# Kernel tuning notes

Hardware: AMD Instinct MI355X
Metric: run time of the kernel (lower is better)

Reference implementation:

```python
import jax, jax.numpy as jnp
import numpy as np
import math

B, S, D = 2, 2048, 1024
H, HKV, HD = 16, 4, 64
SF = 4
SD = HD // SF  # sparsity proj dim = 16
TEMP = 1.0
INIT_STD = 0.02


def rope(qk):
    # qk: [b, h, s, d]
    d = qk.shape[-1]
    theta = 1.0 / (10000.0 ** (jnp.arange(0, d, 2, dtype=jnp.float32) / d))  # [d/2]
    s = jnp.arange(qk.shape[2], dtype=jnp.float32)
    freqs = jnp.outer(s, theta)                     # [s, d/2]
    freqs = jnp.concatenate([freqs, freqs], -1)     # [s, d]
    qk1, qk2 = jnp.split(qk, 2, axis=-1)
    rot = jnp.concatenate([-qk2, qk1], -1)
    return qk * jnp.cos(freqs) + rot * jnp.sin(freqs)


def setup_inputs() -> dict:
    key = jax.random.key(0)
    ks = jax.random.split(key, 8)
    x = jax.random.normal(ks[0], (B, S, D), dtype=jnp.float32)
    Wq = jax.random.normal(ks[1], (D, D), dtype=jnp.float32) * INIT_STD
    Wk = jax.random.normal(ks[2], (HKV * HD, D), dtype=jnp.float32) * INIT_STD
    Wv = jax.random.normal(ks[3], (HKV * HD, D), dtype=jnp.float32) * INIT_STD
    Wo = jax.random.normal(ks[4], (D, D), dtype=jnp.float32) * INIT_STD
    bo = jnp.zeros((D,), dtype=jnp.float32)
    Ws = jax.random.normal(ks[5], (SD, HD), dtype=jnp.float32) * INIT_STD
    bs = jnp.zeros((SD,), dtype=jnp.float32)
    return {"x": x, "Wq": Wq, "Wk": Wk, "Wv": Wv, "Wo": Wo, "bo": bo, "Ws": Ws, "bs": bs}


def reference(x, Wq, Wk, Wv, Wo, bo, Ws, bs):
    b, s, _ = x.shape
    # projections (torch Linear: x @ W.T)
    q = (x @ Wq.T).reshape(b, s, H, HD).transpose(0, 2, 1, 3)     # [b,H,s,hd]
    k = (x @ Wk.T).reshape(b, s, HKV, HD).transpose(0, 2, 1, 3)   # [b,Hkv,s,hd]
    v = (x @ Wv.T).reshape(b, s, HKV, HD).transpose(0, 2, 1, 3)
    q = rope(q)
    k = rope(k)
    n_rep = H // HKV
    k = jnp.repeat(k, n_rep, axis=1)  # [b,H,s,hd]
    v = jnp.repeat(v, n_rep, axis=1)
    # low-rank sparsity gate
    q_sp = q @ Ws.T + bs              # [b,H,s,sd]
    k_sp = k @ Ws.T + bs
    sp_scores = jnp.einsum('bhid,bhjd->bhij', q_sp, k_sp) / math.sqrt(SD)
    gate = jax.nn.sigmoid(sp_scores / TEMP)
    attn = jnp.einsum('bhid,bhjd->bhij', q, k) / math.sqrt(HD)
    attn = attn * gate
    causal = jnp.triu(jnp.ones((s, s), dtype=bool), k=1)
    attn = jnp.where(causal, -jnp.inf, attn)
    w = jax.nn.softmax(attn, axis=-1)
    out = jnp.einsum('bhij,bhjd->bhid', w, v)               # [b,H,s,hd]
    out = out.transpose(0, 2, 1, 3).reshape(b, s, H * HD)   # [b,s,D]
    return out @ Wo.T + bo
```

## Files before the change

kernel.cpp:

```cpp
#include <hip/hip_runtime.h>
#include <math.h>

#define B_ 2
#define S_ 2048
#define D_ 1024
#define H_ 16
#define HKV_ 4
#define HD_ 64
#define SD_ 16

typedef __attribute__((ext_vector_type(8))) short bf16x8;
typedef __attribute__((ext_vector_type(4))) float f32x4;
typedef __attribute__((ext_vector_type(8))) unsigned short us8;
typedef __attribute__((ext_vector_type(4))) unsigned short us4;

#define LOG2E 1.4426950408889634f

__device__ __forceinline__ unsigned short f2bf(float f) {
  unsigned int u = __builtin_bit_cast(unsigned int, f);
  u += 0x7fffu + ((u >> 16) & 1u);
  return (unsigned short)(u >> 16);
}

__device__ __forceinline__ void gload16(const unsigned short* g, unsigned short* l) {
  __builtin_amdgcn_global_load_lds(
      (const __attribute__((address_space(1))) unsigned int*)g,
      (__attribute__((address_space(3))) unsigned int*)l, 16, 0, 0);
}

__global__ __launch_bounds__(256) void convert_bf16(
    const float* __restrict__ x, const float* __restrict__ wq,
    const float* __restrict__ wk, const float* __restrict__ wv,
    const float* __restrict__ wo, unsigned short* __restrict__ xb,
    unsigned short* __restrict__ wqkv, unsigned short* __restrict__ wob) {
  const int blk = blockIdx.x;
  const float* src;
  unsigned short* dst;
  int off;
  if (blk < 2048)      { src = x;  dst = xb;             off = blk * 2048; }
  else if (blk < 2560) { src = wq; dst = wqkv;           off = (blk - 2048) * 2048; }
  else if (blk < 2688) { src = wk; dst = wqkv + 1048576; off = (blk - 2560) * 2048; }
  else if (blk < 2816) { src = wv; dst = wqkv + 1310720; off = (blk - 2688) * 2048; }
  else                 { src = wo; dst = wob;            off = (blk - 2816) * 2048; }
  const int i = off + threadIdx.x * 8;
  float4 a = *(const float4*)(src + i);
  float4 b = *(const float4*)(src + i + 4);
  us8 o;
  o[0] = f2bf(a.x); o[1] = f2bf(a.y); o[2] = f2bf(a.z); o[3] = f2bf(a.w);
  o[4] = f2bf(b.x); o[5] = f2bf(b.y); o[6] = f2bf(b.z); o[7] = f2bf(b.w);
  *(us8*)(dst + i) = o;
}

__global__ __launch_bounds__(256) void gemm_bf16(
    const unsigned short* __restrict__ A, const unsigned short* __restrict__ Bm,
    const float* __restrict__ bias, float* __restrict__ C, int N) {
  __shared__ unsigned short As[64 * 64];
  __shared__ unsigned short Bs[128 * 64];
  const int tid = threadIdx.x;
  const int w = tid >> 6, lane = tid & 63;
  const int nm = lane & 15, quad = lane >> 4;
  const int m0 = blockIdx.y * 64, n0 = blockIdx.x * 128;
  const int wn = w * 32;

  f32x4 acc[4][2] = {};
  int arow[2], acol[2], brow[4], bcol[4];
#pragma unroll
  for (int it = 0; it < 2; ++it) {
    int s = it * 256 + tid;
    arow[it] = s >> 3;
    acol[it] = ((s & 7) ^ (arow[it] & 7)) * 8;
  }
#pragma unroll
  for (int it = 0; it < 4; ++it) {
    int s = it * 256 + tid;
    brow[it] = s >> 3;
    bcol[it] = ((s & 7) ^ (brow[it] & 7)) * 8;
  }

  for (int k0 = 0; k0 < 1024; k0 += 64) {
    __syncthreads();
#pragma unroll
    for (int it = 0; it < 2; ++it)
      gload16(A + (size_t)(m0 + arow[it]) * 1024 + k0 + acol[it],
              &As[(it * 256 + w * 64) * 8]);
#pragma unroll
    for (int it = 0; it < 4; ++it)
      gload16(Bm + (size_t)(n0 + brow[it]) * 1024 + k0 + bcol[it],
              &Bs[(it * 256 + w * 64) * 8]);
    __syncthreads();

#pragma unroll
    for (int ks = 0; ks < 2; ++ks) {
      const int cq = ks * 4 + quad;
      bf16x8 af[4], bfr[2];
#pragma unroll
      for (int mi = 0; mi < 4; ++mi) {
        const int m = mi * 16 + nm;
        af[mi] = *(const bf16x8*)&As[(m * 8 + (cq ^ (m & 7))) * 8];
      }
#pragma unroll
      for (int ni = 0; ni < 2; ++ni) {
        const int n = wn + ni * 16 + nm;
        bfr[ni] = *(const bf16x8*)&Bs[(n * 8 + (cq ^ (n & 7))) * 8];
      }
#pragma unroll
      for (int mi = 0; mi < 4; ++mi)
#pragma unroll
        for (int ni = 0; ni < 2; ++ni)
          acc[mi][ni] = __builtin_amdgcn_mfma_f32_16x16x32_bf16(
              af[mi], bfr[ni], acc[mi][ni], 0, 0, 0);
    }
  }

  float bv[2] = {0.f, 0.f};
  if (bias) {
#pragma unroll
    for (int ni = 0; ni < 2; ++ni) bv[ni] = bias[n0 + wn + ni * 16 + nm];
  }
#pragma unroll
  for (int mi = 0; mi < 4; ++mi) {
#pragma unroll
    for (int r = 0; r < 4; ++r) {
      const int row = m0 + mi * 16 + quad * 4 + r;
      float* crow = C + (size_t)row * N + n0 + wn + nm;
#pragma unroll
      for (int ni = 0; ni < 2; ++ni) crow[ni * 16] = acc[mi][ni][r] + bv[ni];
    }
  }
}

__global__ __launch_bounds__(256) void rope_scatter(
    const float* __restrict__ P, const float* __restrict__ Ws,
    const float* __restrict__ bs, unsigned short* __restrict__ qh,
    unsigned short* __restrict__ kh, unsigned short* __restrict__ qsp,
    unsigned short* __restrict__ ksp) {
  __shared__ float wsl[16 * 64];
  __shared__ float bsl[16];
  __shared__ float rbuf[4][64];
  const int tid = threadIdx.x;
  const int row = blockIdx.x;
  const int b = row >> 11;
  const int s = row & 2047;
  {
    *(float4*)&wsl[tid * 4] = *(const float4*)&Ws[tid * 4];
    if (tid < 16) bsl[tid] = bs[tid];
  }
  __syncthreads();
  const int w = tid >> 6, lane = tid & 63;
  const int i = lane & 31, halfu = lane >> 5;
  const float theta = powf(10000.f, -((float)(2 * i) * (1.f / 64.f)));
  const float f = (float)s * theta;
  const float cf = cosf(f);
  const float sf = sinf(f);
  for (int slot = w; slot < 20; slot += 4) {
    float val = P[(size_t)row * 1536 + slot * 64 + lane];
    float partner = __shfl_xor(val, 32);
    float rot = halfu ? partner : -partner;
    float r = val * cf + rot * sf;
    unsigned short* dst;
    unsigned short* spdst;
    float qscale, spscale;
    if (slot < 16) {
      dst = qh + ((size_t)(b * 16 + slot) * 2048 + s) * 64;
      spdst = qsp + ((size_t)(b * 16 + slot) * 2048 + s) * 16;
      qscale = 0.125f * LOG2E; spscale = 0.25f * LOG2E;
    } else {
      int hh = slot - 16;
      dst = kh + ((size_t)(b * 4 + hh) * 2048 + s) * 64;
      spdst = ksp + ((size_t)(b * 4 + hh) * 2048 + s) * 16;
      qscale = 1.f; spscale = 1.f;
    }
    dst[lane] = f2bf(r * qscale);
    rbuf[w][lane] = r;
    int p = lane >> 4, j = lane & 15;
    float partial = 0.f;
#pragma unroll
    for (int t = 0; t < 16; ++t)
      partial += wsl[j * 64 + p * 16 + t] * rbuf[w][p * 16 + t];
    partial += __shfl_xor(partial, 16);
    partial += __shfl_xor(partial, 32);
    if (p == 0) spdst[j] = f2bf((partial + bsl[j]) * spscale);
  }
}

__global__ __launch_bounds__(256) void v_transpose(
    const float* __restrict__ proj, unsigned short* __restrict__ vt) {
  __shared__ unsigned short t_[64 * 72];
  const int bkv = blockIdx.y;
  const int s0 = blockIdx.x * 64;
  const int b = bkv >> 2, hkv = bkv & 3;
  const int tid = threadIdx.x;
  const int sl = tid >> 2;
  const int c0 = (tid & 3) * 16;
  const float* src = proj + ((size_t)b * 2048 + s0 + sl) * 1536 + 1280 + hkv * 64 + c0;
  us8 o0, o1;
#pragma unroll
  for (int t = 0; t < 8; ++t) { o0[t] = f2bf(src[t]); o1[t] = f2bf(src[8 + t]); }
  *(us8*)&t_[sl * 72 + c0] = o0;
  *(us8*)&t_[sl * 72 + c0 + 8] = o1;
  __syncthreads();
  const int d = tid >> 2;
  const int sc_ = (tid & 3) * 16;
  us8 w0, w1;
#pragma unroll
  for (int t = 0; t < 8; ++t) w0[t] = t_[(sc_ + t) * 72 + d];
#pragma unroll
  for (int t = 0; t < 8; ++t) w1[t] = t_[(sc_ + 8 + t) * 72 + d];
  unsigned short* dst = vt + (size_t)bkv * 131072 + (size_t)d * 2048 + s0 + sc_;
  *(us8*)dst = w0;
  *(us8*)(dst + 8) = w1;
}

template <bool MASK>
__device__ __forceinline__ void attn_tile(
    const unsigned short* __restrict__ Ksb, const unsigned short* __restrict__ Vsb,
    const unsigned short* __restrict__ Kspb_, unsigned short* __restrict__ pt,
    bf16x8 qa0, bf16x8 qa1, bf16x8 qspa, int j0, int qrow0, int nm, int quad,
    int ws, float& l_q, f32x4 O[4]) {
#pragma unroll
  for (int stl = 0; stl < 2; ++stl) {
    const int st = ws * 2 + stl;
    const int kg0 = j0 + st * 16;
    unsigned short* wptr = &pt[nm * 32 + (((stl * 4 + quad) ^ (nm & 6)) * 4)];
    if (MASK && (kg0 > qrow0 + 15)) {
      uint2 zz; zz.x = 0u; zz.y = 0u;
      *(uint2*)wptr = zz;
      continue;
    }
    const int krow = st * 16 + nm;
    const int r7 = krow & 7;
    bf16x8 kb0 = *(const bf16x8*)&Ksb[(krow * 8 + (quad ^ r7)) * 8];
    bf16x8 kb1 = *(const bf16x8*)&Ksb[(krow * 8 + ((4 + quad) ^ r7)) * 8];
    bf16x8 gb = *(const bf16x8*)&Kspb_[(krow * 2 + (quad & 1)) * 8];
    f32x4 z = {0.f, 0.f, 0.f, 0.f};
    f32x4 s = __builtin_amdgcn_mfma_f32_16x16x32_bf16(kb0, qa0, z, 0, 0, 0);
    s = __builtin_amdgcn_mfma_f32_16x16x32_bf16(kb1, qa1, s, 0, 0, 0);
    f32x4 g = __builtin_amdgcn_mfma_f32_16x16x32_bf16(gb, qspa, z, 0, 0, 0);
    const int qv = qrow0 + nm;
    float p0, p1, p2, p3;
#pragma unroll
    for (int r = 0; r < 4; ++r) {
      float gate = __builtin_amdgcn_rcpf(1.f + __builtin_amdgcn_exp2f(-g[r]));
      float v = s[r] * gate;
      if (MASK && (kg0 + 15 > qrow0)) {
        const int key = kg0 + quad * 4 + r;
        v = (key > qv) ? -INFINITY : v;
      }
      float p = __builtin_amdgcn_exp2f(v);
      l_q += p;
      if (r == 0) p0 = p; else if (r == 1) p1 = p; else if (r == 2) p2 = p; else p3 = p;
    }
    unsigned int u0 = (unsigned int)f2bf(p0) | ((unsigned int)f2bf(p1) << 16);
    unsigned int u1 = (unsigned int)f2bf(p2) | ((unsigned int)f2bf(p3) << 16);
    uint2 pk; pk.x = u0; pk.y = u1;
    *(uint2*)wptr = pk;
  }

  bf16x8 pa = *(const bf16x8*)&pt[nm * 32 + (((quad * 2) ^ (nm & 6)) * 4)];
#pragma unroll
  for (int dt = 0; dt < 4; ++dt) {
    const int vrow = dt * 16 + nm;
    bf16x8 vb = *(const bf16x8*)&Vsb[(vrow * 8 + ((ws * 4 + quad) ^ (vrow & 7))) * 8];
    O[dt] = __builtin_amdgcn_mfma_f32_16x16x32_bf16(pa, vb, O[dt], 0, 0, 0);
  }
}

__global__ __launch_bounds__(512) void attn_kernel(
    const unsigned short* __restrict__ qh, const unsigned short* __restrict__ kh,
    const unsigned short* __restrict__ vt, const unsigned short* __restrict__ qsp,
    const unsigned short* __restrict__ ksp, unsigned short* __restrict__ ao) {
  __shared__ unsigned short Ks[2][64 * 64];
  __shared__ unsigned short Vs[2][64 * 64];
  __shared__ unsigned short Ksp[2][64 * 16];
  __shared__ unsigned short Pt[8][512];
  __shared__ float Ox[4][16][64];
  __shared__ float Lxs[4][2][16];

  const int tid = threadIdx.x;
  const int w = tid >> 6;
  const int ws = w >> 2;
  const int wr = w & 3;
  const int lane = tid & 63;
  const int nm = lane & 15;
  const int quad = lane >> 4;
  const int bh = blockIdx.y;
  const int b = bh >> 4, h = bh & 15;
  const int hkv = h >> 2;
  const size_t kbase = (size_t)(b * 4 + hkv) * 2048 * 64;
  const size_t vbase = (size_t)(b * 4 + hkv) * 131072;
  const size_t kspb = (size_t)(b * 4 + hkv) * 2048 * 16;

  const int Lc = tid;
  const int sr = Lc >> 3;
  const int sc = ((Lc & 7) ^ (sr & 7)) * 8;
  unsigned short* pt = &Pt[w][0];

#define STAGE(BUF, J0)                                                         \
  {                                                                            \
    gload16(kh + kbase + (size_t)((J0) + sr) * 64 + sc,                        \
            &Ks[BUF][(w * 64) * 8]);                                           \
    gload16(vt + vbase + (size_t)sr * 2048 + (J0) + sc,                        \
            &Vs[BUF][(w * 64) * 8]);                                           \
    if (w < 2) {                                                               \
      gload16(ksp + kspb + (size_t)((J0) + (Lc >> 1)) * 16 + (Lc & 1) * 8,     \
              &Ksp[BUF][w * 512]);                                             \
    }                                                                          \
  }

  const int qxA = 31 - blockIdx.x;
  const int qxB = blockIdx.x;
  const int qrow0A = qxA * 64 + wr * 16;
  const int qrow0B = qxB * 64 + wr * 16;

  const size_t qbA = ((size_t)(b * 16 + h) * 2048 + qrow0A + nm) * 64;
  bf16x8 qa0A = *(const bf16x8*)(qh + qbA + quad * 8);
  bf16x8 qa1A = *(const bf16x8*)(qh + qbA + 32 + quad * 8);
  const size_t qbB = ((size_t)(b * 16 + h) * 2048 + qrow0B + nm) * 64;
  bf16x8 qa0B = *(const bf16x8*)(qh + qbB + quad * 8);
  bf16x8 qa1B = *(const bf16x8*)(qh + qbB + 32 + quad * 8);
  bf16x8 qspaA = {0, 0, 0, 0, 0, 0, 0, 0};
  bf16x8 qspaB = {0, 0, 0, 0, 0, 0, 0, 0};
  if (quad < 2) {
    qspaA = *(const bf16x8*)(qsp + ((size_t)(b * 16 + h) * 2048 + qrow0A + nm) * 16 + quad * 8);
    qspaB = *(const bf16x8*)(qsp + ((size_t)(b * 16 + h) * 2048 + qrow0B + nm) * 16 + quad * 8);
  }

  float l_q = 0.f;
  f32x4 O[4] = {{0.f, 0.f, 0.f, 0.f}, {0.f, 0.f, 0.f, 0.f},
                {0.f, 0.f, 0.f, 0.f}, {0.f, 0.f, 0.f, 0.f}};

  STAGE(0, 0);
  int cur = 0;
  for (int jt = 0; jt < qxA; ++jt) {
    __syncthreads();
    STAGE(cur ^ 1, (jt + 1) * 64)
    attn_tile<false>(&Ks[cur][0], &Vs[cur][0], &Ksp[cur][0], pt,
                     qa0A, qa1A, qspaA, jt * 64, qrow0A, nm, quad, ws, l_q, O);
    cur ^= 1;
  }
  __syncthreads();
  STAGE(cur ^ 1, 0)
  attn_tile<true>(&Ks[cur][0], &Vs[cur][0], &Ksp[cur][0], pt,
                  qa0A, qa1A, qspaA, qxA * 64, qrow0A, nm, quad, ws, l_q, O);
  cur ^= 1;

  {
    float lsum = l_q;
    lsum += __shfl_xor(lsum, 16);
    lsum += __shfl_xor(lsum, 32);
    if (quad == 0) Lxs[wr][ws][nm] = lsum;
  }
  if (ws == 1) {
#pragma unroll
    for (int dt = 0; dt < 4; ++dt)
#pragma unroll
      for (int r = 0; r < 4; ++r) Ox[wr][dt * 4 + r][lane] = O[dt][r];
  }
  __syncthreads();
  if (ws == 0) {
#pragma unroll
    for (int r = 0; r < 4; ++r) {
      const float tot = Lxs[wr][0][quad * 4 + r] + Lxs[wr][1][quad * 4 + r];
      const float inv = __builtin_amdgcn_rcpf(tot);
      const int rowg = qrow0A + quad * 4 + r;
      unsigned short* orow = ao + ((size_t)b * 2048 + rowg) * 1024 + h * 64 + nm;
#pragma unroll
      for (int dt = 0; dt < 4; ++dt)
        orow[dt * 16] = f2bf((O[dt][r] + Ox[wr][dt * 4 + r][lane]) * inv);
    }
  }
#pragma unroll
  for (int dt = 0; dt < 4; ++dt) O[dt] = (f32x4){0.f, 0.f, 0.f, 0.f};
  l_q = 0.f;

  for (int jt = 0; jt < qxB; ++jt) {
    __syncthreads();
    STAGE(cur ^ 1, (jt + 1) * 64)
    attn_tile<false>(&Ks[cur][0], &Vs[cur][0], &Ksp[cur][0], pt,
                     qa0B, qa1B, qspaB, jt * 64, qrow0B, nm, quad, ws, l_q, O);
    cur ^= 1;
  }
  __syncthreads();
  attn_tile<true>(&Ks[cur][0], &Vs[cur][0], &Ksp[cur][0], pt,
                  qa0B, qa1B, qspaB, qxB * 64, qrow0B, nm, quad, ws, l_q, O);

  {
    float lsum = l_q;
    lsum += __shfl_xor(lsum, 16);
    lsum += __shfl_xor(lsum, 32);
    if (quad == 0) Lxs[wr][ws][nm] = lsum;
  }
  if (ws == 1) {
#pragma unroll
    for (int dt = 0; dt < 4; ++dt)
#pragma unroll
      for (int r = 0; r < 4; ++r) Ox[wr][dt * 4 + r][lane] = O[dt][r];
  }
  __syncthreads();
  if (ws == 0) {
#pragma unroll
    for (int r = 0; r < 4; ++r) {
      const float tot = Lxs[wr][0][quad * 4 + r] + Lxs[wr][1][quad * 4 + r];
      const float inv = __builtin_amdgcn_rcpf(tot);
      const int rowg = qrow0B + quad * 4 + r;
      unsigned short* orow = ao + ((size_t)b * 2048 + rowg) * 1024 + h * 64 + nm;
#pragma unroll
      for (int dt = 0; dt < 4; ++dt)
        orow[dt * 16] = f2bf((O[dt][r] + Ox[wr][dt * 4 + r][lane]) * inv);
    }
  }
#undef STAGE
}

extern "C" void kernel_launch(void* const* d_in, const int* in_sizes, int n_in,
                              void* d_out, int out_size, void* d_ws,
                              size_t ws_size, hipStream_t stream) {
  const float* x = (const float*)d_in[0];
  const float* Wq = (const float*)d_in[1];
  const float* Wk = (const float*)d_in[2];
  const float* Wv = (const float*)d_in[3];
  const float* Wo = (const float*)d_in[4];
  const float* bo = (const float*)d_in[5];
  const float* Ws = (const float*)d_in[6];
  const float* bs = (const float*)d_in[7];
  float* out = (float*)d_out;

  char* wsb = (char*)d_ws;
  float* proj = (float*)wsb;
  unsigned short* aob  = (unsigned short*)wsb;
  unsigned short* qh   = (unsigned short*)(wsb + 25165824);
  unsigned short* kh   = (unsigned short*)(wsb + 33554432);
  unsigned short* vtb  = (unsigned short*)(wsb + 35651584);
  unsigned short* qsp  = (unsigned short*)(wsb + 37748736);
  unsigned short* ksp  = (unsigned short*)(wsb + 39845888);
  unsigned short* xb   = (unsigned short*)(wsb + 40370176);
  unsigned short* wqkv = (unsigned short*)(wsb + 48758784);
  unsigned short* wob  = (unsigned short*)(wsb + 51904512);

  convert_bf16<<<dim3(3328), 256, 0, stream>>>(x, Wq, Wk, Wv, Wo, xb, wqkv, wob);
  gemm_bf16<<<dim3(12, 64), 256, 0, stream>>>(xb, wqkv, nullptr, proj, 1536);
  rope_scatter<<<dim3(4096), 256, 0, stream>>>(proj, Ws, bs, qh, kh, qsp, ksp);
  v_transpose<<<dim3(32, 8), 256, 0, stream>>>(proj, vtb);
  attn_kernel<<<dim3(16, 32), 512, 0, stream>>>(qh, kh, vtb, qsp, ksp, aob);
  gemm_bf16<<<dim3(8, 64), 256, 0, stream>>>(aob, wob, bo, out, 1024);
}
```

Baseline: 189.4 us.

## Triple-buffer K/V staging with vmcnt waits and fuse both query-tile loops

Replaces the double-buffered K/V/Ksp staging with a three-stage ring and merges the two query-tile passes into one 33-iteration loop, so loads run two tiles ahead across the pass boundary. Waiting on outstanding loads now uses explicit s_waitcnt vmcnt counts plus a raw s_barrier instead of __syncthreads. The Ox cross-wave reduction buffer is dropped and its data written into the consumed K/V slot, which offsets the extra LDS taken by the third stage. The hand-tuned vmcnt counts depend on exactly how many loads each wave issues per STAGE, so they are fragile if the load mix changes.

```diff
diff --git a/kernel.cpp b/kernel.cpp
--- a/kernel.cpp
+++ b/kernel.cpp
@@ -269,11 +269,10 @@
     const unsigned short* __restrict__ qh, const unsigned short* __restrict__ kh,
     const unsigned short* __restrict__ vt, const unsigned short* __restrict__ qsp,
     const unsigned short* __restrict__ ksp, unsigned short* __restrict__ ao) {
-  __shared__ unsigned short Ks[2][64 * 64];
-  __shared__ unsigned short Vs[2][64 * 64];
-  __shared__ unsigned short Ksp[2][64 * 16];
+  __shared__ unsigned short Ks[3][64 * 64];
+  __shared__ unsigned short Vs[3][64 * 64];
+  __shared__ unsigned short Ksp[3][64 * 16];
   __shared__ unsigned short Pt[8][512];
-  __shared__ float Ox[4][16][64];
   __shared__ float Lxs[4][2][16];
 
   const int tid = threadIdx.x;
@@ -330,83 +329,95 @@
                 {0.f, 0.f, 0.f, 0.f}, {0.f, 0.f, 0.f, 0.f}};
 
   STAGE(0, 0);
-  int cur = 0;
-  for (int jt = 0; jt < qxA; ++jt) {
+  STAGE(1, 64);
+  for (int i = 0; i < 33; ++i) {
+    if (w < 2) { asm volatile("s_waitcnt vmcnt(3)" ::: "memory"); }
+    else       { asm volatile("s_waitcnt vmcnt(2)" ::: "memory"); }
+    __builtin_amdgcn_s_barrier();
+    if (i + 2 < 33) {
+      const int i2 = i + 2;
+      const int j2 = (i2 <= qxA ? i2 : i2 - qxA - 1) * 64;
+      STAGE(i2 % 3, j2);
+    }
+    const int cur = i % 3;
+    if (i == qxA) {
+      attn_tile<true>(&Ks[cur][0], &Vs[cur][0], &Ksp[cur][0], pt,
+                      qa0A, qa1A, qspaA, qxA * 64, qrow0A, nm, quad, ws, l_q, O);
+      __syncthreads();
+      float* oxk = (float*)&Ks[cur][0];
+      float* oxv = (float*)&Vs[cur][0];
+      float* ox = (wr & 2) ? oxv : oxk;
+      {
+        float lsum = l_q;
+        lsum += __shfl_xor(lsum, 16);
+        lsum += __shfl_xor(lsum, 32);
+        if (quad == 0) Lxs[wr][ws][nm] = lsum;
+      }
+      if (ws == 1) {
+#pragma unroll
+        for (int dt = 0; dt < 4; ++dt)
+#pragma unroll
+          for (int r = 0; r < 4; ++r)
+            ox[(wr & 1) * 1024 + (dt * 4 + r) * 64 + lane] = O[dt][r];
+      }
+      __syncthreads();
+      if (ws == 0) {
+#pragma unroll
+        for (int r = 0; r < 4; ++r) {
+          const float tot = Lxs[wr][0][quad * 4 + r] + Lxs[wr][1][quad * 4 + r];
+          const float inv = __builtin_amdgcn_rcpf(tot);
+          const int rowg = qrow0A + quad * 4 + r;
+          unsigned short* orow = ao + ((size_t)b * 2048 + rowg) * 1024 + h * 64 + nm;
+#pragma unroll
+          for (int dt = 0; dt < 4; ++dt)
+            orow[dt * 16] = f2bf((O[dt][r] + ox[(wr & 1) * 1024 + (dt * 4 + r) * 64 + lane]) * inv);
+        }
+      }
+#pragma unroll
+      for (int dt = 0; dt < 4; ++dt) O[dt] = (f32x4){0.f, 0.f, 0.f, 0.f};
+      l_q = 0.f;
+    } else if (i == 32) {
+      attn_tile<true>(&Ks[cur][0], &Vs[cur][0], &Ksp[cur][0], pt,
+                      qa0B, qa1B, qspaB, qxB * 64, qrow0B, nm, quad, ws, l_q, O);
+    } else if (i < qxA) {
+      attn_tile<false>(&Ks[cur][0], &Vs[cur][0], &Ksp[cur][0], pt,
+                       qa0A, qa1A, qspaA, i * 64, qrow0A, nm, quad, ws, l_q, O);
+    } else {
+      attn_tile<false>(&Ks[cur][0], &Vs[cur][0], &Ksp[cur][0], pt,
+                       qa0B, qa1B, qspaB, (i - qxA - 1) * 64, qrow0B, nm, quad, ws, l_q, O);
+    }
+  }
+
+  __syncthreads();
+  {
+    float* oxk = (float*)&Ks[2][0];
+    float* oxv = (float*)&Vs[2][0];
+    float* ox = (wr & 2) ? oxv : oxk;
+    {
+      float lsum = l_q;
+      lsum += __shfl_xor(lsum, 16);
+      lsum += __shfl_xor(lsum, 32);
+      if (quad == 0) Lxs[wr][ws][nm] = lsum;
+    }
+    if (ws == 1) {
+#pragma unroll
+      for (int dt = 0; dt < 4; ++dt)
+#pragma unroll
+        for (int r = 0; r < 4; ++r)
+          ox[(wr & 1) * 1024 + (dt * 4 + r) * 64 + lane] = O[dt][r];
+    }
     __syncthreads();
-    STAGE(cur ^ 1, (jt + 1) * 64)
-    attn_tile<false>(&Ks[cur][0], &Vs[cur][0], &Ksp[cur][0], pt,
-                     qa0A, qa1A, qspaA, jt * 64, qrow0A, nm, quad, ws, l_q, O);
-    cur ^= 1;
-  }
-  __syncthreads();
-  STAGE(cur ^ 1, 0)
-  attn_tile<true>(&Ks[cur][0], &Vs[cur][0], &Ksp[cur][0], pt,
-                  qa0A, qa1A, qspaA, qxA * 64, qrow0A, nm, quad, ws, l_q, O);
-  cur ^= 1;
-
-  {
-    float lsum = l_q;
-    lsum += __shfl_xor(lsum, 16);
-    lsum += __shfl_xor(lsum, 32);
-    if (quad == 0) Lxs[wr][ws][nm] = lsum;
-  }
-  if (ws == 1) {
-#pragma unroll
-    for (int dt = 0; dt < 4; ++dt)
-#pragma unroll
-      for (int r = 0; r < 4; ++r) Ox[wr][dt * 4 + r][lane] = O[dt][r];
-  }
-  __syncthreads();
-  if (ws == 0) {
-#pragma unroll
-    for (int r = 0; r < 4; ++r) {
-      const float tot = Lxs[wr][0][quad * 4 + r] + Lxs[wr][1][quad * 4 + r];
-      const float inv = __builtin_amdgcn_rcpf(tot);
-      const int rowg = qrow0A + quad * 4 + r;
-      unsigned short* orow = ao + ((size_t)b * 2048 + rowg) * 1024 + h * 64 + nm;
-#pragma unroll
-      for (int dt = 0; dt < 4; ++dt)
-        orow[dt * 16] = f2bf((O[dt][r] + Ox[wr][dt * 4 + r][lane]) * inv);
-    }
-  }
-#pragma unroll
-  for (int dt = 0; dt < 4; ++dt) O[dt] = (f32x4){0.f, 0.f, 0.f, 0.f};
-  l_q = 0.f;
-
-  for (int jt = 0; jt < qxB; ++jt) {
-    __syncthreads();
-    STAGE(cur ^ 1, (jt + 1) * 64)
-    attn_tile<false>(&Ks[cur][0], &Vs[cur][0], &Ksp[cur][0], pt,
-                     qa0B, qa1B, qspaB, jt * 64, qrow0B, nm, quad, ws, l_q, O);
-    cur ^= 1;
-  }
-  __syncthreads();
-  attn_tile<true>(&Ks[cur][0], &Vs[cur][0], &Ksp[cur][0], pt,
-                  qa0B, qa1B, qspaB, qxB * 64, qrow0B, nm, quad, ws, l_q, O);
-
-  {
-    float lsum = l_q;
-    lsum += __shfl_xor(lsum, 16);
-    lsum += __shfl_xor(lsum, 32);
-    if (quad == 0) Lxs[wr][ws][nm] = lsum;
-  }
-  if (ws == 1) {
-#pragma unroll
-    for (int dt = 0; dt < 4; ++dt)
-#pragma unroll
-      for (int r = 0; r < 4; ++r) Ox[wr][dt * 4 + r][lane] = O[dt][r];
-  }
-  __syncthreads();
-  if (ws == 0) {
-#pragma unroll
-    for (int r = 0; r < 4; ++r) {
-      const float tot = Lxs[wr][0][quad * 4 + r] + Lxs[wr][1][quad * 4 + r];
-      const float inv = __builtin_amdgcn_rcpf(tot);
-      const int rowg = qrow0B + quad * 4 + r;
-      unsigned short* orow = ao + ((size_t)b * 2048 + rowg) * 1024 + h * 64 + nm;
-#pragma unroll
-      for (int dt = 0; dt < 4; ++dt)
-        orow[dt * 16] = f2bf((O[dt][r] + Ox[wr][dt * 4 + r][lane]) * inv);
+    if (ws == 0) {
+#pragma unroll
+      for (int r = 0; r < 4; ++r) {
+        const float tot = Lxs[wr][0][quad * 4 + r] + Lxs[wr][1][quad * 4 + r];
+        const float inv = __builtin_amdgcn_rcpf(tot);
+        const int rowg = qrow0B + quad * 4 + r;
+        unsigned short* orow = ao + ((size_t)b * 2048 + rowg) * 1024 + h * 64 + nm;
+#pragma unroll
+        for (int dt = 0; dt < 4; ++dt)
+          orow[dt * 16] = f2bf((O[dt][r] + ox[(wr & 1) * 1024 + (dt * 4 + r) * 64 + lane]) * inv);
+      }
     }
   }
 #undef STAGE
```

After: 220.2 us. 16.2% more time.

## Split key tile across four waves per row group and drop P LDS roundtrip

Applied to the files above, without the earlier changes.

Attention blocks grow from 512 to 1024 threads, so each of four wave groups handles 16 keys of every 64-key tile instead of 32. The P tile now feeds the PV product straight from registers through a 16x16x16 bf16 MFMA, which removes the per-wave LDS staging buffer. K/Ksp and V staging are split between separate wave halves, and partial O sums are merged with LDS atomics. This aims at more parallelism and fewer LDS transfers, at the cost of smaller MFMAs, LDS atomic contention and heavier register pressure under the new launch bounds.

```diff
diff --git a/kernel.cpp b/kernel.cpp
--- a/kernel.cpp
+++ b/kernel.cpp
@@ -10,6 +10,7 @@
 #define SD_ 16
 
 typedef __attribute__((ext_vector_type(8))) short bf16x8;
+typedef __attribute__((ext_vector_type(4))) short bf16x4;
 typedef __attribute__((ext_vector_type(4))) float f32x4;
 typedef __attribute__((ext_vector_type(8))) unsigned short us8;
 typedef __attribute__((ext_vector_type(4))) unsigned short us4;
@@ -214,67 +215,56 @@
 template <bool MASK>
 __device__ __forceinline__ void attn_tile(
     const unsigned short* __restrict__ Ksb, const unsigned short* __restrict__ Vsb,
-    const unsigned short* __restrict__ Kspb_, unsigned short* __restrict__ pt,
+    const unsigned short* __restrict__ Kspb_,
     bf16x8 qa0, bf16x8 qa1, bf16x8 qspa, int j0, int qrow0, int nm, int quad,
     int ws, float& l_q, f32x4 O[4]) {
-#pragma unroll
-  for (int stl = 0; stl < 2; ++stl) {
-    const int st = ws * 2 + stl;
-    const int kg0 = j0 + st * 16;
-    unsigned short* wptr = &pt[nm * 32 + (((stl * 4 + quad) ^ (nm & 6)) * 4)];
-    if (MASK && (kg0 > qrow0 + 15)) {
-      uint2 zz; zz.x = 0u; zz.y = 0u;
-      *(uint2*)wptr = zz;
-      continue;
-    }
-    const int krow = st * 16 + nm;
-    const int r7 = krow & 7;
-    bf16x8 kb0 = *(const bf16x8*)&Ksb[(krow * 8 + (quad ^ r7)) * 8];
-    bf16x8 kb1 = *(const bf16x8*)&Ksb[(krow * 8 + ((4 + quad) ^ r7)) * 8];
-    bf16x8 gb = *(const bf16x8*)&Kspb_[(krow * 2 + (quad & 1)) * 8];
-    f32x4 z = {0.f, 0.f, 0.f, 0.f};
-    f32x4 s = __builtin_amdgcn_mfma_f32_16x16x32_bf16(kb0, qa0, z, 0, 0, 0);
-    s = __builtin_amdgcn_mfma_f32_16x16x32_bf16(kb1, qa1, s, 0, 0, 0);
-    f32x4 g = __builtin_amdgcn_mfma_f32_16x16x32_bf16(gb, qspa, z, 0, 0, 0);
-    const int qv = qrow0 + nm;
-    float p0, p1, p2, p3;
-#pragma unroll
-    for (int r = 0; r < 4; ++r) {
-      float gate = __builtin_amdgcn_rcpf(1.f + __builtin_amdgcn_exp2f(-g[r]));
-      float v = s[r] * gate;
-      if (MASK && (kg0 + 15 > qrow0)) {
-        const int key = kg0 + quad * 4 + r;
-        v = (key > qv) ? -INFINITY : v;
-      }
-      float p = __builtin_amdgcn_exp2f(v);
-      l_q += p;
-      if (r == 0) p0 = p; else if (r == 1) p1 = p; else if (r == 2) p2 = p; else p3 = p;
-    }
-    unsigned int u0 = (unsigned int)f2bf(p0) | ((unsigned int)f2bf(p1) << 16);
-    unsigned int u1 = (unsigned int)f2bf(p2) | ((unsigned int)f2bf(p3) << 16);
-    uint2 pk; pk.x = u0; pk.y = u1;
-    *(uint2*)wptr = pk;
-  }
-
-  bf16x8 pa = *(const bf16x8*)&pt[nm * 32 + (((quad * 2) ^ (nm & 6)) * 4)];
+  const int kg0 = j0 + ws * 16;
+  if (MASK && (kg0 > qrow0 + 15)) return;
+
+  const int krow = ws * 16 + nm;
+  const int r7 = krow & 7;
+  bf16x8 kb0 = *(const bf16x8*)&Ksb[(krow * 8 + (quad ^ r7)) * 8];
+  bf16x8 kb1 = *(const bf16x8*)&Ksb[(krow * 8 + ((4 + quad) ^ r7)) * 8];
+  bf16x8 gb = *(const bf16x8*)&Kspb_[(krow * 2 + (quad & 1)) * 8];
+  f32x4 z = {0.f, 0.f, 0.f, 0.f};
+  f32x4 s = __builtin_amdgcn_mfma_f32_16x16x32_bf16(kb0, qa0, z, 0, 0, 0);
+  s = __builtin_amdgcn_mfma_f32_16x16x32_bf16(kb1, qa1, s, 0, 0, 0);
+  f32x4 g = __builtin_amdgcn_mfma_f32_16x16x32_bf16(gb, qspa, z, 0, 0, 0);
+  const int qv = qrow0 + nm;
+  f32x4 ps;
+#pragma unroll
+  for (int r = 0; r < 4; ++r) {
+    float gate = __builtin_amdgcn_rcpf(1.f + __builtin_amdgcn_exp2f(-g[r]));
+    float v = s[r] * gate;
+    if (MASK && (kg0 + 15 > qrow0)) {
+      const int key = kg0 + quad * 4 + r;
+      v = (key > qv) ? -INFINITY : v;
+    }
+    float p = __builtin_amdgcn_exp2f(v);
+    l_q += p;
+    ps[r] = p;
+  }
+  bf16x4 pa;
+  pa[0] = (short)f2bf(ps[0]); pa[1] = (short)f2bf(ps[1]);
+  pa[2] = (short)f2bf(ps[2]); pa[3] = (short)f2bf(ps[3]);
+  const int c = ws * 2 + (quad >> 1);
 #pragma unroll
   for (int dt = 0; dt < 4; ++dt) {
     const int vrow = dt * 16 + nm;
-    bf16x8 vb = *(const bf16x8*)&Vsb[(vrow * 8 + ((ws * 4 + quad) ^ (vrow & 7))) * 8];
-    O[dt] = __builtin_amdgcn_mfma_f32_16x16x32_bf16(pa, vb, O[dt], 0, 0, 0);
-  }
-}
-
-__global__ __launch_bounds__(512) void attn_kernel(
+    bf16x4 vb = *(const bf16x4*)&Vsb[(vrow * 8 + (c ^ (vrow & 7))) * 8 + (quad & 1) * 4];
+    O[dt] = __builtin_amdgcn_mfma_f32_16x16x16bf16_1k(pa, vb, O[dt], 0, 0, 0);
+  }
+}
+
+__global__ __launch_bounds__(1024, 8) void attn_kernel(
     const unsigned short* __restrict__ qh, const unsigned short* __restrict__ kh,
     const unsigned short* __restrict__ vt, const unsigned short* __restrict__ qsp,
     const unsigned short* __restrict__ ksp, unsigned short* __restrict__ ao) {
   __shared__ unsigned short Ks[2][64 * 64];
   __shared__ unsigned short Vs[2][64 * 64];
   __shared__ unsigned short Ksp[2][64 * 16];
-  __shared__ unsigned short Pt[8][512];
   __shared__ float Ox[4][16][64];
-  __shared__ float Lxs[4][2][16];
+  __shared__ float Lxs[4][4][16];
 
   const int tid = threadIdx.x;
   const int w = tid >> 6;
@@ -290,20 +280,21 @@
   const size_t vbase = (size_t)(b * 4 + hkv) * 131072;
   const size_t kspb = (size_t)(b * 4 + hkv) * 2048 * 16;
 
-  const int Lc = tid;
+  const int Lc = tid & 511;
   const int sr = Lc >> 3;
   const int sc = ((Lc & 7) ^ (sr & 7)) * 8;
-  unsigned short* pt = &Pt[w][0];
 
 #define STAGE(BUF, J0)                                                         \
   {                                                                            \
-    gload16(kh + kbase + (size_t)((J0) + sr) * 64 + sc,                        \
-            &Ks[BUF][(w * 64) * 8]);                                           \
-    gload16(vt + vbase + (size_t)sr * 2048 + (J0) + sc,                        \
-            &Vs[BUF][(w * 64) * 8]);                                           \
-    if (w < 2) {                                                               \
-      gload16(ksp + kspb + (size_t)((J0) + (Lc >> 1)) * 16 + (Lc & 1) * 8,     \
-              &Ksp[BUF][w * 512]);                                             \
+    if (w < 8) {                                                               \
+      gload16(kh + kbase + (size_t)((J0) + sr) * 64 + sc,                      \
+              &Ks[BUF][(w * 64) * 8]);                                         \
+      if (w < 2)                                                               \
+        gload16(ksp + kspb + (size_t)((J0) + (tid >> 1)) * 16 + (tid & 1) * 8, \
+                &Ksp[BUF][w * 512]);                                           \
+    } else {                                                                   \
+      gload16(vt + vbase + (size_t)sr * 2048 + (J0) + sc,                      \
+              &Vs[BUF][((w - 8) * 64) * 8]);                                   \
     }                                                                          \
   }
 
@@ -334,13 +325,13 @@
   for (int jt = 0; jt < qxA; ++jt) {
     __syncthreads();
     STAGE(cur ^ 1, (jt + 1) * 64)
-    attn_tile<false>(&Ks[cur][0], &Vs[cur][0], &Ksp[cur][0], pt,
+    attn_tile<false>(&Ks[cur][0], &Vs[cur][0], &Ksp[cur][0],
                      qa0A, qa1A, qspaA, jt * 64, qrow0A, nm, quad, ws, l_q, O);
     cur ^= 1;
   }
   __syncthreads();
   STAGE(cur ^ 1, 0)
-  attn_tile<true>(&Ks[cur][0], &Vs[cur][0], &Ksp[cur][0], pt,
+  attn_tile<true>(&Ks[cur][0], &Vs[cur][0], &Ksp[cur][0],
                   qa0A, qa1A, qspaA, qxA * 64, qrow0A, nm, quad, ws, l_q, O);
   cur ^= 1;
 
@@ -350,23 +341,31 @@
     lsum += __shfl_xor(lsum, 32);
     if (quad == 0) Lxs[wr][ws][nm] = lsum;
   }
-  if (ws == 1) {
+  if (ws == 0) {
 #pragma unroll
     for (int dt = 0; dt < 4; ++dt)
 #pragma unroll
       for (int r = 0; r < 4; ++r) Ox[wr][dt * 4 + r][lane] = O[dt][r];
   }
   __syncthreads();
+  if (ws != 0) {
+#pragma unroll
+    for (int dt = 0; dt < 4; ++dt)
+#pragma unroll
+      for (int r = 0; r < 4; ++r) atomicAdd(&Ox[wr][dt * 4 + r][lane], O[dt][r]);
+  }
+  __syncthreads();
   if (ws == 0) {
 #pragma unroll
     for (int r = 0; r < 4; ++r) {
-      const float tot = Lxs[wr][0][quad * 4 + r] + Lxs[wr][1][quad * 4 + r];
+      const int q = quad * 4 + r;
+      const float tot = Lxs[wr][0][q] + Lxs[wr][1][q] + Lxs[wr][2][q] + Lxs[wr][3][q];
       const float inv = __builtin_amdgcn_rcpf(tot);
-      const int rowg = qrow0A + quad * 4 + r;
+      const int rowg = qrow0A + q;
       unsigned short* orow = ao + ((size_t)b * 2048 + rowg) * 1024 + h * 64 + nm;
 #pragma unroll
       for (int dt = 0; dt < 4; ++dt)
-        orow[dt * 16] = f2bf((O[dt][r] + Ox[wr][dt * 4 + r][lane]) * inv);
+        orow[dt * 16] = f2bf(Ox[wr][dt * 4 + r][lane] * inv);
     }
   }
 #pragma unroll
@@ -376,12 +375,12 @@
   for (int jt = 0; jt < qxB; ++jt) {
     __syncthreads();
     STAGE(cur ^ 1, (jt + 1) * 64)
-    attn_tile<false>(&Ks[cur][0], &Vs[cur][0], &Ksp[cur][0], pt,
+    attn_tile<false>(&Ks[cur][0], &Vs[cur][0], &Ksp[cur][0],
                      qa0B, qa1B, qspaB, jt * 64, qrow0B, nm, quad, ws, l_q, O);
     cur ^= 1;
   }
   __syncthreads();
-  attn_tile<true>(&Ks[cur][0], &Vs[cur][0], &Ksp[cur][0], pt,
+  attn_tile<true>(&Ks[cur][0], &Vs[cur][0], &Ksp[cur][0],
                   qa0B, qa1B, qspaB, qxB * 64, qrow0B, nm, quad, ws, l_q, O);
 
   {
@@ -390,23 +389,31 @@
     lsum += __shfl_xor(lsum, 32);
     if (quad == 0) Lxs[wr][ws][nm] = lsum;
   }
-  if (ws == 1) {
+  if (ws == 0) {
 #pragma unroll
     for (int dt = 0; dt < 4; ++dt)
 #pragma unroll
       for (int r = 0; r < 4; ++r) Ox[wr][dt * 4 + r][lane] = O[dt][r];
   }
   __syncthreads();
+  if (ws != 0) {
+#pragma unroll
+    for (int dt = 0; dt < 4; ++dt)
+#pragma unroll
+      for (int r = 0; r < 4; ++r) atomicAdd(&Ox[wr][dt * 4 + r][lane], O[dt][r]);
+  }
+  __syncthreads();
   if (ws == 0) {
 #pragma unroll
     for (int r = 0; r < 4; ++r) {
-      const float tot = Lxs[wr][0][quad * 4 + r] + Lxs[wr][1][quad * 4 + r];
+      const int q = quad * 4 + r;
+      const float tot = Lxs[wr][0][q] + Lxs[wr][1][q] + Lxs[wr][2][q] + Lxs[wr][3][q];
       const float inv = __builtin_amdgcn_rcpf(tot);
-      const int rowg = qrow0B + quad * 4 + r;
+      const int rowg = qrow0B + q;
       unsigned short* orow = ao + ((size_t)b * 2048 + rowg) * 1024 + h * 64 + nm;
 #pragma unroll
       for (int dt = 0; dt < 4; ++dt)
-        orow[dt * 16] = f2bf((O[dt][r] + Ox[wr][dt * 4 + r][lane]) * inv);
+        orow[dt * 16] = f2bf(Ox[wr][dt * 4 + r][lane] * inv);
     }
   }
 #undef STAGE
@@ -441,6 +448,6 @@
   gemm_bf16<<<dim3(12, 64), 256, 0, stream>>>(xb, wqkv, nullptr, proj, 1536);
   rope_scatter<<<dim3(4096), 256, 0, stream>>>(proj, Ws, bs, qh, kh, qsp, ksp);
   v_transpose<<<dim3(32, 8), 256, 0, stream>>>(proj, vtb);
-  attn_kernel<<<dim3(16, 32), 512, 0, stream>>>(qh, kh, vtb, qsp, ksp, aob);
+  attn_kernel<<<dim3(16, 32), 1024, 0, stream>>>(qh, kh, vtb, qsp, ksp, aob);
   gemm_bf16<<<dim3(8, 64), 256, 0, stream>>>(aob, wob, bo, out, 1024);
 }
```

New measurement: 282.1 us. 48.9% more time.
